# Performance work log

Hardware: AMD Instinct MI355X
Metric: run time of the kernel (lower is better)

## Reference

```python
import jax, jax.numpy as jnp
import numpy as np
from jax.scipy.special import ndtri
from jax.scipy.stats import norm

MU = 0.0
SIGMA = 1.0
K = 128
B, N = 64, 4096
_P_EPS = 1e-7  # keep inverse-CDF argument strictly inside (0,1)


def setup_inputs() -> dict:
    key = jax.random.key(0)
    k1, k2, k3 = jax.random.split(key, 3)
    C = jax.random.randint(k1, (B, N), 0, K, dtype=jnp.int64)
    eps = jax.random.normal(k2, (B, N), dtype=jnp.float32)
    U = jax.random.uniform(k3, (B, N, K), dtype=jnp.float32)
    return {"C": C, "eps": eps, "U": U}


def reference(C, eps, U):
    # upper bounds: u ~ Normal(mu, sigma), reparameterized via eps
    u = MU + SIGMA * eps                      # [B, N]
    # truncated standard normal on (-inf, u] via inverse CDF:
    #   z = Phi^{-1}(U * Phi(u))
    p = U * norm.cdf(u)[..., None]            # [B, N, K]
    z = ndtri(jnp.clip(p, _P_EPS, 1.0 - _P_EPS))
    # scatter: Z[b, i, C[b, i]] = u[b, i]
    onehot = jax.nn.one_hot(C, K, dtype=jnp.bool_)  # [B, N, K]
    Z = jnp.where(onehot, u[..., None], z)
    return Z
```

## Files before the change

kernel.cpp:

```cpp
#include <hip/hip_runtime.h>
#include <math.h>

typedef float f32x4 __attribute__((ext_vector_type(4)));

__device__ __forceinline__ float ndtri_as(float p) {
    bool hi = p >= 0.5f;
    float pp = hi ? (1.0f - p) : p;
    float t = __fsqrt_rn(-1.38629436112f * __log2f(pp));
    float num = fmaf(fmaf(0.010328f, t, 0.802853f), t, 2.515517f);
    float den = fmaf(fmaf(fmaf(0.001308f, t, 0.189269f), t, 1.432788f), t, 1.0f);
    float z = t - num * __builtin_amdgcn_rcpf(den);
    return hi ? z : -z;
}

__device__ __forceinline__ float elem(float uval, float cdfu, float u, bool is_c) {
    const float PLO  = 1e-7f;
    const float PHI_ = 1.0f - 1e-7f;
    float p = fminf(fmaxf(uval * cdfu, PLO), PHI_);
    float z = ndtri_as(p);
    return is_c ? u : z;
}

__device__ __forceinline__ f32x4 quad(f32x4 uv, float cdfu, float u, int k0, int c) {
    f32x4 r;
    r.x = elem(uv.x, cdfu, u, (k0 + 0) == c);
    r.y = elem(uv.y, cdfu, u, (k0 + 1) == c);
    r.z = elem(uv.z, cdfu, u, (k0 + 2) == c);
    r.w = elem(uv.w, cdfu, u, (k0 + 3) == c);
    return r;
}

__global__ __launch_bounds__(256) void phi_kernel(
    const float* __restrict__ eps, float* __restrict__ cdfu, int n)
{
    int i = blockIdx.x * blockDim.x + threadIdx.x;
    if (i < n) cdfu[i] = normcdff(eps[i]);
}

template <bool USE_WS>
__global__ __launch_bounds__(256) void MappingToContinuous_kernel(
    const int* __restrict__ C,
    const float* __restrict__ eps,
    const float* __restrict__ cdfu_t,
    const f32x4* __restrict__ U,
    f32x4* __restrict__ out)
{
    int i0 = blockIdx.x * 1024 + threadIdx.x;
    int i1 = i0 + 256, i2 = i0 + 512, i3 = i0 + 768;

    f32x4 u0 = U[i0], u1 = U[i1], u2 = U[i2], u3 = U[i3];

    int r0 = i0 >> 5, r1 = i1 >> 5, r2 = i2 >> 5, r3 = i3 >> 5;
    float e0 = eps[r0], e1 = eps[r1], e2 = eps[r2], e3 = eps[r3];
    float f0 = USE_WS ? cdfu_t[r0] : normcdff(e0);
    float f1 = USE_WS ? cdfu_t[r1] : normcdff(e1);
    float f2 = USE_WS ? cdfu_t[r2] : normcdff(e2);
    float f3 = USE_WS ? cdfu_t[r3] : normcdff(e3);
    int c0 = C[r0], c1 = C[r1], c2 = C[r2], c3 = C[r3];

    f32x4 o0 = quad(u0, f0, e0, (i0 & 31) << 2, c0);
    f32x4 o1 = quad(u1, f1, e1, (i1 & 31) << 2, c1);
    f32x4 o2 = quad(u2, f2, e2, (i2 & 31) << 2, c2);
    f32x4 o3 = quad(u3, f3, e3, (i3 & 31) << 2, c3);

    __builtin_nontemporal_store(o0, &out[i0]);
    __builtin_nontemporal_store(o1, &out[i1]);
    __builtin_nontemporal_store(o2, &out[i2]);
    __builtin_nontemporal_store(o3, &out[i3]);
}

extern "C" void kernel_launch(void* const* d_in, const int* in_sizes, int n_in,
                              void* d_out, int out_size, void* d_ws, size_t ws_size,
                              hipStream_t stream) {
    const int*   C   = (const int*)d_in[0];
    const float* eps = (const float*)d_in[1];
    const f32x4* U   = (const f32x4*)d_in[2];
    f32x4* out = (f32x4*)d_out;

    int nrows  = in_sizes[1];
    int total4 = out_size / 4;
    int grid   = total4 / 1024;

    size_t ws_needed = (size_t)nrows * sizeof(float);
    if (ws_size >= ws_needed) {
        float* cdfu = (float*)d_ws;
        hipLaunchKernelGGL(phi_kernel, dim3((nrows + 255) / 256), dim3(256),
                           0, stream, eps, cdfu, nrows);
        hipLaunchKernelGGL((MappingToContinuous_kernel<true>), dim3(grid), dim3(256),
                           0, stream, C, eps, cdfu, U, out);
    } else {
        hipLaunchKernelGGL((MappingToContinuous_kernel<false>), dim3(grid), dim3(256),
                           0, stream, C, eps, (const float*)nullptr, U, out);
    }
}
```

Baseline: 49.44 us.

## Fuse Phi precompute into main kernel via per-block shared row params

Removes the separate phi_kernel launch and its workspace round-trip. Each block now covers 64 rows (2048 float4s); 64 threads load eps and C for those rows and compute normcdf once, sharing the results through LDS after a barrier. Each thread now issues eight float4 loads instead of four, which gives more memory-level parallelism but raises register use and halves the grid.

```diff
diff --git a/kernel.cpp b/kernel.cpp
--- a/kernel.cpp
+++ b/kernel.cpp
@@ -30,43 +30,57 @@
     return r;
 }
 
-__global__ __launch_bounds__(256) void phi_kernel(
-    const float* __restrict__ eps, float* __restrict__ cdfu, int n)
-{
-    int i = blockIdx.x * blockDim.x + threadIdx.x;
-    if (i < n) cdfu[i] = normcdff(eps[i]);
-}
-
-template <bool USE_WS>
 __global__ __launch_bounds__(256) void MappingToContinuous_kernel(
     const int* __restrict__ C,
     const float* __restrict__ eps,
-    const float* __restrict__ cdfu_t,
     const f32x4* __restrict__ U,
     f32x4* __restrict__ out)
 {
-    int i0 = blockIdx.x * 1024 + threadIdx.x;
-    int i1 = i0 + 256, i2 = i0 + 512, i3 = i0 + 768;
+    __shared__ float e_s[64];
+    __shared__ float f_s[64];
+    __shared__ int   c_s[64];
 
-    f32x4 u0 = U[i0], u1 = U[i1], u2 = U[i2], u3 = U[i3];
+    int t  = threadIdx.x;
+    int i0 = blockIdx.x * 2048 + t;
 
-    int r0 = i0 >> 5, r1 = i1 >> 5, r2 = i2 >> 5, r3 = i3 >> 5;
-    float e0 = eps[r0], e1 = eps[r1], e2 = eps[r2], e3 = eps[r3];
-    float f0 = USE_WS ? cdfu_t[r0] : normcdff(e0);
-    float f1 = USE_WS ? cdfu_t[r1] : normcdff(e1);
-    float f2 = USE_WS ? cdfu_t[r2] : normcdff(e2);
-    float f3 = USE_WS ? cdfu_t[r3] : normcdff(e3);
-    int c0 = C[r0], c1 = C[r1], c2 = C[r2], c3 = C[r3];
+    f32x4 u0 = U[i0];
+    f32x4 u1 = U[i0 +  256];
+    f32x4 u2 = U[i0 +  512];
+    f32x4 u3 = U[i0 +  768];
+    f32x4 u4 = U[i0 + 1024];
+    f32x4 u5 = U[i0 + 1280];
+    f32x4 u6 = U[i0 + 1536];
+    f32x4 u7 = U[i0 + 1792];
 
-    f32x4 o0 = quad(u0, f0, e0, (i0 & 31) << 2, c0);
-    f32x4 o1 = quad(u1, f1, e1, (i1 & 31) << 2, c1);
-    f32x4 o2 = quad(u2, f2, e2, (i2 & 31) << 2, c2);
-    f32x4 o3 = quad(u3, f3, e3, (i3 & 31) << 2, c3);
+    int row0 = blockIdx.x * 64;
+    if (t < 64) {
+        float e = eps[row0 + t];
+        e_s[t] = e;
+        f_s[t] = normcdff(e);
+        c_s[t] = C[row0 + t];
+    }
+    __syncthreads();
 
-    __builtin_nontemporal_store(o0, &out[i0]);
-    __builtin_nontemporal_store(o1, &out[i1]);
-    __builtin_nontemporal_store(o2, &out[i2]);
-    __builtin_nontemporal_store(o3, &out[i3]);
+    int lr = t >> 5;
+    int k0 = (t & 31) << 2;
+
+    f32x4 o;
+    o = quad(u0, f_s[lr +  0], e_s[lr +  0], k0, c_s[lr +  0]);
+    __builtin_nontemporal_store(o, &out[i0]);
+    o = quad(u1, f_s[lr +  8], e_s[lr +  8], k0, c_s[lr +  8]);
+    __builtin_nontemporal_store(o, &out[i0 +  256]);
+    o = quad(u2, f_s[lr + 16], e_s[lr + 16], k0, c_s[lr + 16]);
+    __builtin_nontemporal_store(o, &out[i0 +  512]);
+    o = quad(u3, f_s[lr + 24], e_s[lr + 24], k0, c_s[lr + 24]);
+    __builtin_nontemporal_store(o, &out[i0 +  768]);
+    o = quad(u4, f_s[lr + 32], e_s[lr + 32], k0, c_s[lr + 32]);
+    __builtin_nontemporal_store(o, &out[i0 + 1024]);
+    o = quad(u5, f_s[lr + 40], e_s[lr + 40], k0, c_s[lr + 40]);
+    __builtin_nontemporal_store(o, &out[i0 + 1280]);
+    o = quad(u6, f_s[lr + 48], e_s[lr + 48], k0, c_s[lr + 48]);
+    __builtin_nontemporal_store(o, &out[i0 + 1536]);
+    o = quad(u7, f_s[lr + 56], e_s[lr + 56], k0, c_s[lr + 56]);
+    __builtin_nontemporal_store(o, &out[i0 + 1792]);
 }
 
 extern "C" void kernel_launch(void* const* d_in, const int* in_sizes, int n_in,
@@ -77,19 +91,9 @@
     const f32x4* U   = (const f32x4*)d_in[2];
     f32x4* out = (f32x4*)d_out;
 
-    int nrows  = in_sizes[1];
     int total4 = out_size / 4;
-    int grid   = total4 / 1024;
+    int grid   = total4 / 2048;
 
-    size_t ws_needed = (size_t)nrows * sizeof(float);
-    if (ws_size >= ws_needed) {
-        float* cdfu = (float*)d_ws;
-        hipLaunchKernelGGL(phi_kernel, dim3((nrows + 255) / 256), dim3(256),
-                           0, stream, eps, cdfu, nrows);
-        hipLaunchKernelGGL((MappingToContinuous_kernel<true>), dim3(grid), dim3(256),
-                           0, stream, C, eps, cdfu, U, out);
-    } else {
-        hipLaunchKernelGGL((MappingToContinuous_kernel<false>), dim3(grid), dim3(256),
-                           0, stream, C, eps, (const float*)nullptr, U, out);
-    }
+    hipLaunchKernelGGL(MappingToContinuous_kernel, dim3(grid), dim3(256),
+                       0, stream, C, eps, U, out);
 }
```

New measurement: 45.74 us (median of 2 runs). -7.5%, faster.
